# Performance work log

Measured on AMD Instinct MI355X. Metric: run time of the kernel, lower is better.

Reference implementation:

```python
import jax, jax.numpy as jnp
import numpy as np

# GemNet-OC hyperparameters (match init_kwargs)
CUTOFF = 6.0
NR = 128     # num_radial
NS = 7       # num_spherical
NB = 2       # num_blocks
DA = 256     # emb_size_atom
DE = 512     # emb_size_edge
DT = 64      # emb_size_trip
DC = 16      # emb_size_cbf/rbf
NRES_M = 2   # edge residual layers per block (before+after skip)
NRES_H = 2   # atom residual layers per block (num_atom)
N_ELEM = 119
INV_SQRT2 = 0.7071067811865476
_GAMMA = 0.5 / (CUTOFF / NR) ** 2  # gaussian rbf width


def _radial_basis(d):
    """Gaussian RBF with polynomial envelope (exponent 5). d: [E] -> [E, NR]."""
    u = d / CUTOFF
    p = 5.0
    env = 1.0 - (p + 1) * (p + 2) / 2 * u**5 + p * (p + 2) * u**6 - p * (p + 1) / 2 * u**7
    env = jnp.where(u < 1.0, env, 0.0)
    mu = jnp.linspace(0.0, CUTOFF, NR, dtype=d.dtype)
    return env[:, None] * jnp.exp(-_GAMMA * (d[:, None] - mu) ** 2)


def setup_inputs() -> dict:
    key = jax.random.key(0)
    ks = jax.random.split(key, 32)
    N, E, T = 8000, 100000, 500000

    atomic_numbers = jax.random.randint(ks[0], (N,), 0, N_ELEM)
    edge_index = jax.random.randint(ks[1], (2, E), 0, N)
    distances = jax.random.uniform(ks[2], (E,), jnp.float32, 0.5, CUTOFF)
    id3_ba = jax.random.randint(ks[3], (T,), 0, E)
    id3_ca = jax.random.randint(ks[4], (T,), 0, E)
    cos_angles = jax.random.uniform(ks[5], (T,), jnp.float32, -0.99, 0.99)

    def w(k, shape, fan_in):
        return jax.random.normal(k, shape, jnp.float32) / np.sqrt(fan_in)

    params = dict(
        atom_table=w(ks[6], (N_ELEM, DA), 1.0),
        W_edge=w(ks[7], (2 * DA + NR, DE), 2 * DA + NR), b_edge=jnp.zeros((DE,), jnp.float32),
        W_rbf3=w(ks[8], (NR, DC), NR),
        W_sph=w(ks[9], (NS, DC), NS),
        W_cbf_up=w(ks[10], (DC, DT), DC),
        W_rbf_h=w(ks[11], (NR, DE), NR),
        W_ba=w(ks[12], (NB, DE, DE), DE), b_ba=jnp.zeros((NB, DE), jnp.float32),
        W_down=w(ks[13], (NB, DE, DT), DE),
        W_trip_up=w(ks[14], (NB, DT, DE), DT),
        W_res_m=w(ks[15], (NB, NRES_M, 2, DE, DE), DE), b_res_m=jnp.zeros((NB, NRES_M, 2, DE), jnp.float32),
        W_e2a=w(ks[16], (NB, DE, DA), DE),
        W_res_h=w(ks[17], (NB, NRES_H, 2, DA, DA), DA), b_res_h=jnp.zeros((NB, NRES_H, 2, DA), jnp.float32),
        W_out=w(ks[18], (DA, 1), DA),
    )
    return dict(atomic_numbers=atomic_numbers, edge_index=edge_index, distances=distances,
                id3_ba=id3_ba, id3_ca=id3_ca, cos_angles=cos_angles, **params)


def reference(atomic_numbers, edge_index, distances, id3_ba, id3_ca, cos_angles,
              atom_table, W_edge, b_edge, W_rbf3, W_sph, W_cbf_up, W_rbf_h,
              W_ba, b_ba, W_down, W_trip_up, W_res_m, b_res_m, W_e2a,
              W_res_h, b_res_h, W_out):
    N = atomic_numbers.shape[0]
    E = distances.shape[0]
    silu = jax.nn.silu

    # --- shared basis functions ---
    rbf = _radial_basis(distances)                               # [E, NR]
    theta = jnp.arccos(jnp.clip(cos_angles, -1.0, 1.0))
    sph = jnp.cos(theta[:, None] * jnp.arange(NS, dtype=theta.dtype))  # [T, NS]
    # circular basis embedding: radial part (gathered per triplet) x angular part
    cbf_emb = (rbf @ W_rbf3)[id3_ba] * (sph @ W_sph)             # [T, DC]
    cbf_up = cbf_emb @ W_cbf_up                                  # [T, DT]
    rbf_h = rbf @ W_rbf_h                                        # [E, DE]

    # --- embeddings ---
    src, tgt = edge_index[0], edge_index[1]
    h = atom_table[atomic_numbers]                               # [N, DA]
    m = silu(jnp.concatenate([h[src], h[tgt], rbf], axis=-1) @ W_edge + b_edge)  # [E, DE]

    def residual(x, Wr, br):  # Wr: [2, D, D], br: [2, D]
        y = silu(x @ Wr[0] + br[0])
        y = silu(y @ Wr[1] + br[1])
        return (x + y) * INV_SQRT2

    # --- interaction blocks ---
    for b in range(NB):
        # triplet message passing (edge -> triplet gather, triplet -> edge scatter)
        x_ba = silu(m @ W_ba[b] + b_ba[b]) @ W_down[b]           # [E, DT]
        x3 = jax.ops.segment_sum(x_ba[id3_ba] * cbf_up, id3_ca, num_segments=E)  # [E, DT]
        m = (m + x3 @ W_trip_up[b]) * INV_SQRT2
        for r in range(NRES_M):
            m = residual(m, W_res_m[b, r], b_res_m[b, r])
        # atom update: rbf-scaled edge messages scattered onto target atoms
        h_msg = jax.ops.segment_sum((m * rbf_h) @ W_e2a[b], tgt, num_segments=N)  # [N, DA]
        h = h + h_msg
        for r in range(NRES_H):
            h = residual(h, W_res_h[b, r], b_res_h[b, r])

    # --- extensive energy output ---
    energy = jnp.sum(h @ W_out)
    return energy
```

## Files before the change

kernel.cpp:

```cpp
#include <hip/hip_runtime.h>
#include <hip/hip_bf16.h>
#include <math.h>

#define CUTOFF 6.0f
#define NRAD 128
#define NSPH 7
#define DA 256
#define DE 512
#define DT 64
#define DCB 16
#define INV_SQRT2 0.7071067811865476f
#define RBF_GAMMA 227.55555555555554f

typedef __hip_bfloat16 bf16;
typedef __bf16 bf16v;
typedef bf16v bf16x8 __attribute__((ext_vector_type(8)));
typedef float f32x4 __attribute__((ext_vector_type(4)));

static inline int cdiv(int a, int b) { return (a + b - 1) / b; }

__device__ __forceinline__ float silu_f(float v) {
    return v / (1.0f + __expf(-v));
}

__device__ __forceinline__ float to_f(float v) { return v; }
__device__ __forceinline__ float to_f(bf16 v) { return __bfloat162float(v); }

template<typename T> __device__ __forceinline__ T from_f(float v);
template<> __device__ __forceinline__ float from_f<float>(float v) { return v; }
template<> __device__ __forceinline__ bf16 from_f<bf16>(float v) { return __float2bfloat16(v); }

#if defined(__has_builtin)
#if __has_builtin(__builtin_amdgcn_global_load_lds)
#define HAS_GLD 1
#endif
#endif

#ifdef HAS_GLD
__device__ __forceinline__ void gld16(const bf16* g, bf16* l) {
    __builtin_amdgcn_global_load_lds(
        (const __attribute__((address_space(1))) void*)g,
        (__attribute__((address_space(3))) void*)l, 16, 0, 0);
}
#endif

template<typename TC, typename TD, int GMODE, bool PRE_ADD, bool HAS_BIAS,
         bool ACT, bool POST_ADD, bool POST_MUL>
__global__ __launch_bounds__(512, 6)
void gemm_mfma(const bf16* __restrict__ A, const bf16* __restrict__ A3,
               const bf16* __restrict__ Bt,
               TC* __restrict__ C, const TC* __restrict__ Cin,
               const TD* __restrict__ Dop, const float* __restrict__ bias,
               const int* __restrict__ idx1, const int* __restrict__ idx2,
               int M, int N, int K, int lda, int ldb, float scale)
{
    __shared__ bf16 lds[3 * 8192];
    const int tid = threadIdx.x;

    const int nwg = gridDim.x * gridDim.y;
    const int bid = blockIdx.y * gridDim.x + blockIdx.x;
    const int q = nwg >> 3, r = nwg & 7;
    const int xcd = bid & 7, jj = bid >> 3;
    const int wg = (xcd < r) ? (xcd * (q + 1) + jj) : (r + xcd * q + jj);
    const int bn = (wg % gridDim.x) * 128;
    const int bm = (wg / gridDim.x) * 128;

    const int w   = tid >> 6;
    const int l   = tid & 63;
    const int l16 = l & 15;
    const int lr4 = (l >> 4) * 4;
    const int wr  = (w >> 2) * 64;
    const int wc  = (w & 3) * 32;
    const int koff = (((l >> 4) ^ ((l16 >> 1) & 3)) << 3);

    f32x4 acc[4][2];
#pragma unroll
    for (int i = 0; i < 4; ++i)
#pragma unroll
        for (int j = 0; j < 2; ++j) acc[i][j] = (f32x4){0.f, 0.f, 0.f, 0.f};

    const int csw = (((l & 3) ^ ((l >> 3) & 3)) << 3);
    const int rA = w * 16 + (l >> 2);

    int ar = bm + rA; if (ar >= M) ar = M - 1;
    const bf16* pAa = A + (long)((GMODE >= 2) ? idx1[ar] : ar) * lda + csw;
    const bf16* pAb = (GMODE >= 2) ? (A + (long)idx2[ar] * lda + csw) : pAa;
    const bf16* pAc = (GMODE == 3) ? (A3 + (long)ar * NRAD + csw) : pAa;

    int bc = bn + rA; if (bc >= N) bc = N - 1;
    const bf16* pB = Bt + (long)bc * ldb + csw;

    const int wofs = (w * 16) * 32;

    auto STAGE = [&](int k0, int bo) {
        const bf16* a0;
        if (GMODE == 0) {
            a0 = pAa + k0;
        } else if (GMODE == 2) {
            a0 = (k0 >= DA) ? (pAb + (k0 - DA)) : (pAa + k0);
        } else {
            if (k0 >= 2 * DA)  a0 = pAc + (k0 - 2 * DA);
            else if (k0 >= DA) a0 = pAb + (k0 - DA);
            else               a0 = pAa + k0;
        }
#ifdef HAS_GLD
        gld16(a0, lds + bo + wofs);
        gld16(pB + k0, lds + bo + 4096 + wofs);
#else
        *(uint4*)(lds + bo + (tid >> 2) * 32 + (tid & 3) * 8) = *(const uint4*)a0;
        *(uint4*)(lds + bo + 4096 + (tid >> 2) * 32 + (tid & 3) * 8) = *(const uint4*)(pB + k0);
#endif
    };

    auto COMPUTE = [&](int bo) {
        const bf16* As_ = lds + bo;
        const bf16* Bs_ = lds + bo + 4096;
        bf16x8 bfr[2];
#pragma unroll
        for (int fn = 0; fn < 2; ++fn)
            bfr[fn] = *(const bf16x8*)&Bs_[(wc + fn * 16 + l16) * 32 + koff];
#pragma unroll
        for (int fm = 0; fm < 4; ++fm) {
            bf16x8 af = *(const bf16x8*)&As_[(wr + fm * 16 + l16) * 32 + koff];
            acc[fm][0] = __builtin_amdgcn_mfma_f32_16x16x32_bf16(af, bfr[0], acc[fm][0], 0, 0, 0);
            acc[fm][1] = __builtin_amdgcn_mfma_f32_16x16x32_bf16(af, bfr[1], acc[fm][1], 0, 0, 0);
        }
    };

    const int nt = K >> 5;

#ifdef HAS_GLD
    if (nt > 0) STAGE(0, 0);
    if (nt > 1) STAGE(32, 8192);
    int boC = 0;
    int boS = 16384;
    for (int t = 0; t < nt; ++t) {
        if (t + 2 < nt) STAGE((t + 2) << 5, boS);
        const int rem = nt - 1 - t;
        __builtin_amdgcn_sched_barrier(0);
        if (rem >= 2)      asm volatile("s_waitcnt vmcnt(4)" ::: "memory");
        else if (rem == 1) asm volatile("s_waitcnt vmcnt(2)" ::: "memory");
        else               asm volatile("s_waitcnt vmcnt(0)" ::: "memory");
        __builtin_amdgcn_sched_barrier(0);
        __builtin_amdgcn_s_barrier();
        __builtin_amdgcn_sched_barrier(0);
        COMPUTE(boC);
        __builtin_amdgcn_s_barrier();
        boC += 8192; if (boC > 16384) boC = 0;
        boS += 8192; if (boS > 16384) boS = 0;
    }
#else
    for (int t = 0; t < nt; ++t) {
        STAGE(t << 5, 0);
        __syncthreads();
        COMPUTE(0);
        __syncthreads();
    }
#endif

#pragma unroll
    for (int fm = 0; fm < 4; ++fm) {
#pragma unroll
        for (int fn = 0; fn < 2; ++fn) {
            const int col = bn + wc + fn * 16 + l16;
            if (col < N) {
#pragma unroll
                for (int r4 = 0; r4 < 4; ++r4) {
                    const int row = bm + wr + fm * 16 + lr4 + r4;
                    if (row < M) {
                        float v = acc[fm][fn][r4];
                        if (PRE_ADD)  v += to_f(Cin[(long)row * N + col]);
                        if (HAS_BIAS) v += bias[col];
                        if (ACT)      v = silu_f(v);
                        if (POST_ADD) v += to_f(Dop[(long)row * N + col]);
                        if (POST_MUL) v *= to_f(Dop[(long)row * N + col]);
                        C[(long)row * N + col] = from_f<TC>(v * scale);
                    }
                }
            }
        }
    }
}

__global__ void f2b_kernel(const float* __restrict__ in, bf16* __restrict__ out, long n)
{
    long i = ((long)blockIdx.x * 256 + threadIdx.x) * 4;
    const long stride = (long)gridDim.x * 256 * 4;
    for (; i < n; i += stride) {
        float4 v = *(const float4*)(in + i);
        bf16 o[4] = {__float2bfloat16(v.x), __float2bfloat16(v.y),
                     __float2bfloat16(v.z), __float2bfloat16(v.w)};
        *(ushort4*)(out + i) = *(const ushort4*)o;
    }
}

__global__ __launch_bounds__(256)
void t2bT_kernel(const float* __restrict__ in, bf16* __restrict__ out, int K, int Nc)
{
    __shared__ float tile[32][33];
    const long bofs = (long)blockIdx.z * K * Nc;
    const int k0 = blockIdx.y * 32;
    const int n0 = blockIdx.x * 32;
    const int tx = threadIdx.x & 31;
    const int ty = threadIdx.x >> 5;
#pragma unroll
    for (int i = 0; i < 4; ++i) {
        int k = k0 + ty + 8 * i;
        tile[ty + 8 * i][tx] = (k < K && n0 + tx < Nc) ? in[bofs + (long)k * Nc + n0 + tx] : 0.f;
    }
    __syncthreads();
#pragma unroll
    for (int i = 0; i < 4; ++i) {
        int n = n0 + ty + 8 * i;
        if (n < Nc && k0 + tx < K)
            out[bofs + (long)n * K + k0 + tx] = from_f<bf16>(tile[tx][ty + 8 * i]);
    }
}

__global__ __launch_bounds__(128)
void basis_kernel(const float* __restrict__ dist,
                  const float* __restrict__ W_rbf3,
                  bf16* __restrict__ rbf, bf16* __restrict__ rbf3, int E)
{
    __shared__ float s_rbf[NRAD];
    const int e = blockIdx.x;
    if (e >= E) return;
    const int k = threadIdx.x;
    const float d = dist[e];
    const float u = d * (1.0f / CUTOFF);
    float u2 = u * u, u4 = u2 * u2, u5 = u4 * u, u6 = u5 * u, u7 = u6 * u;
    float env = 1.0f - 21.0f * u5 + 35.0f * u6 - 15.0f * u7;
    if (u >= 1.0f) env = 0.0f;
    const float mu = CUTOFF * (float)k / (float)(NRAD - 1);
    const float t = d - mu;
    const float v = env * __expf(-RBF_GAMMA * t * t);
    s_rbf[k] = v;
    rbf[(long)e * NRAD + k] = __float2bfloat16(v);
    __syncthreads();

    if (k < DCB) {
        float acc = 0.f;
        for (int kk = 0; kk < NRAD; ++kk) acc += s_rbf[kk] * W_rbf3[kk * DCB + k];
        rbf3[(long)e * DCB + k] = __float2bfloat16(acc);
    }
}

__global__ void h_init_kernel(const int* __restrict__ an,
                              const float* __restrict__ table,
                              float* __restrict__ h, int N)
{
    int i = blockIdx.x * 256 + threadIdx.x;
    if (i < N * DA) {
        int a = i >> 8;
        int c = i & 255;
        h[i] = table[(long)an[a] * DA + c];
    }
}

__global__ void zeroi_kernel(int* __restrict__ p, int n)
{
    int i = blockIdx.x * 256 + threadIdx.x;
    if (i < n) p[i] = 0;
}
__global__ void copyi_kernel(const int* __restrict__ a, int* __restrict__ b, int n)
{
    int i = blockIdx.x * 256 + threadIdx.x;
    if (i < n) b[i] = a[i];
}
__global__ void count_kernel(const int* __restrict__ idx, int* __restrict__ cnt, int n)
{
    int i = blockIdx.x * 256 + threadIdx.x;
    if (i < n) atomicAdd(&cnt[idx[i]], 1);
}
__global__ __launch_bounds__(256)
void seg_p1(const int* __restrict__ cnt, int* __restrict__ bsum, int n)
{
    __shared__ int s[256];
    int i = blockIdx.x * 256 + threadIdx.x;
    s[threadIdx.x] = (i < n) ? cnt[i] : 0;
    __syncthreads();
    for (int o = 128; o > 0; o >>= 1) {
        if (threadIdx.x < o) s[threadIdx.x] += s[threadIdx.x + o];
        __syncthreads();
    }
    if (threadIdx.x == 0) bsum[blockIdx.x] = s[0];
}
__global__ __launch_bounds__(1024)
void seg_p2(int* __restrict__ bsum, int* __restrict__ off, int nb, int n)
{
    __shared__ int s[1024];
    int v = (threadIdx.x < nb) ? bsum[threadIdx.x] : 0;
    s[threadIdx.x] = v;
    __syncthreads();
    for (int o = 1; o < 1024; o <<= 1) {
        int t = (threadIdx.x >= o) ? s[threadIdx.x - o] : 0;
        __syncthreads();
        s[threadIdx.x] += t;
        __syncthreads();
    }
    if (threadIdx.x < nb) bsum[threadIdx.x] = s[threadIdx.x] - v;
    if (threadIdx.x == nb - 1) off[n] = s[threadIdx.x];
}
__global__ __launch_bounds__(256)
void seg_p3(const int* __restrict__ cnt, const int* __restrict__ bsum,
            int* __restrict__ off, int n)
{
    __shared__ int s[256];
    int i = blockIdx.x * 256 + threadIdx.x;
    int v = (i < n) ? cnt[i] : 0;
    s[threadIdx.x] = v;
    __syncthreads();
    for (int o = 1; o < 256; o <<= 1) {
        int t = (threadIdx.x >= o) ? s[threadIdx.x - o] : 0;
        __syncthreads();
        s[threadIdx.x] += t;
        __syncthreads();
    }
    if (i < n) off[i] = bsum[blockIdx.x] + s[threadIdx.x] - v;
}
__global__ void fill_kernel(const int* __restrict__ idx, int* __restrict__ cur,
                            int* __restrict__ list, int n)
{
    int i = blockIdx.x * 256 + threadIdx.x;
    if (i < n) {
        int p = atomicAdd(&cur[idx[i]], 1);
        list[p] = i;
    }
}

__global__ __launch_bounds__(256)
void emb16_kernel(const float* __restrict__ cosang,
                  const int* __restrict__ id3_ba,
                  const bf16* __restrict__ rbf3,
                  const float* __restrict__ W_sph,
                  bf16* __restrict__ emb, int T)
{
    __shared__ float s_W[NSPH * DCB];
    const int tid = threadIdx.x;
    if (tid < NSPH * DCB) s_W[tid] = W_sph[tid];
    __syncthreads();
    const long idx = (long)blockIdx.x * 256 + tid;
    if (idx >= (long)T * DCB) return;
    const int t = (int)(idx >> 4);
    const int cc = (int)(idx & 15);
    float c = cosang[t];
    c = fminf(1.0f, fmaxf(-1.0f, c));
    float s0 = 1.0f, s1 = c;
    float a = s_W[0 * DCB + cc] + c * s_W[1 * DCB + cc];
#pragma unroll
    for (int s = 2; s < NSPH; ++s) {
        float s2 = 2.0f * c * s1 - s0;
        a += s2 * s_W[s * DCB + cc];
        s0 = s1; s1 = s2;
    }
    emb[idx] = __float2bfloat16(a * to_f(rbf3[(long)id3_ba[t] * DCB + cc]));
}

__global__ __launch_bounds__(256)
void x3_gather_kernel(const int* __restrict__ ca_off, const int* __restrict__ ca_list,
                      const int* __restrict__ id3_ba,
                      const bf16* __restrict__ emb, const bf16* __restrict__ xba,
                      const float* __restrict__ W_up,
                      bf16* __restrict__ x3, int E)
{
    __shared__ float s_Wup[DCB * DT];
    const int tid = threadIdx.x;
    for (int i = tid; i < DCB * DT; i += 256) s_Wup[i] = W_up[i];
    __syncthreads();
    const int e = blockIdx.x * 4 + (tid >> 6);
    const int d = tid & 63;
    if (e >= E) return;
    const int j0 = ca_off[e], j1 = ca_off[e + 1];
    float acc = 0.f;
    for (int j = j0; j < j1; ++j) {
        const int t = ca_list[j];
        const int ba = id3_ba[t];
        const ushort* ep = (const ushort*)(emb + (long)t * DCB);
        float dotv = 0.f;
#pragma unroll
        for (int cc = 0; cc < DCB; ++cc)
            dotv += __uint_as_float((unsigned)ep[cc] << 16) * s_Wup[cc * DT + d];
        acc += dotv * to_f(xba[(long)ba * DT + d]);
    }
    x3[(long)e * DT + d] = from_f<bf16>(acc);
}

__global__ __launch_bounds__(256)
void atom_segsum_kernel(const int* __restrict__ tgt_off, const int* __restrict__ tgt_list,
                        const bf16* __restrict__ g, bf16* __restrict__ s_out, int N)
{
    const int a = blockIdx.x;
    if (a >= N) return;
    const int c = threadIdx.x;
    float acc0 = 0.f, acc1 = 0.f;
    const int j0 = tgt_off[a], j1 = tgt_off[a + 1];
    for (int j = j0; j < j1; ++j) {
        const bf16* row = g + (long)tgt_list[j] * DE;
        acc0 += to_f(row[c]);
        acc1 += to_f(row[c + 256]);
    }
    s_out[(long)a * DE + c]       = from_f<bf16>(acc0);
    s_out[(long)a * DE + c + 256] = from_f<bf16>(acc1);
}

__global__ __launch_bounds__(256)
void reduce1_kernel(const float* __restrict__ h, const float* __restrict__ Wout,
                    float* __restrict__ partials, int N)
{
    __shared__ float s[256];
    const int a0 = blockIdx.x * 32;
    const int col = threadIdx.x;
    float acc = 0.f;
    for (int a = 0; a < 32; ++a) {
        int row = a0 + a;
        if (row < N) acc += h[(long)row * DA + col];
    }
    acc *= Wout[col];
    s[col] = acc;
    __syncthreads();
    for (int off = 128; off > 0; off >>= 1) {
        if (col < off) s[col] += s[col + off];
        __syncthreads();
    }
    if (col == 0) partials[blockIdx.x] = s[0];
}

__global__ __launch_bounds__(256)
void reduce2_kernel(const float* __restrict__ partials, float* __restrict__ out, int nb)
{
    __shared__ float s[256];
    float acc = 0.f;
    for (int i = threadIdx.x; i < nb; i += 256) acc += partials[i];
    s[threadIdx.x] = acc;
    __syncthreads();
    for (int off = 128; off > 0; off >>= 1) {
        if (threadIdx.x < off) s[threadIdx.x] += s[threadIdx.x + off];
        __syncthreads();
    }
    if (threadIdx.x == 0) out[0] = s[0];
}

__global__ void diag_kernel(float* out, float v) { out[0] = v; }

extern "C" void kernel_launch(void* const* d_in, const int* in_sizes, int n_in,
                              void* d_out, int out_size, void* d_ws, size_t ws_size,
                              hipStream_t stream)
{
    const int*   atomic_numbers = (const int*)d_in[0];
    const int*   edge_index     = (const int*)d_in[1];
    const float* distances      = (const float*)d_in[2];
    const int*   id3_ba         = (const int*)d_in[3];
    const int*   id3_ca         = (const int*)d_in[4];
    const float* cos_angles     = (const float*)d_in[5];
    const float* atom_table     = (const float*)d_in[6];
    const float* W_edge         = (const float*)d_in[7];
    const float* b_edge         = (const float*)d_in[8];
    const float* W_rbf3         = (const float*)d_in[9];
    const float* W_sph          = (const float*)d_in[10];
    const float* W_cbf_up       = (const float*)d_in[11];
    const float* W_rbf_h        = (const float*)d_in[12];
    const float* W_ba           = (const float*)d_in[13];
    const float* b_ba           = (const float*)d_in[14];
    const float* W_down         = (const float*)d_in[15];
    const float* W_trip_up      = (const float*)d_in[16];
    const float* W_res_m        = (const float*)d_in[17];
    const float* b_res_m        = (const float*)d_in[18];
    const float* W_e2a          = (const float*)d_in[19];
    const float* W_res_h        = (const float*)d_in[20];
    const float* b_res_h        = (const float*)d_in[21];
    const float* W_out          = (const float*)d_in[22];

    const int N = in_sizes[0];
    const int E = in_sizes[2];
    const int T = in_sizes[3];
    const int* src = edge_index;
    const int* tgt = edge_index + E;

    char* base = (char*)d_ws;
    size_t off = 0;
    auto alloc = [&](size_t bytes) -> void* {
        void* r = base + off;
        off += (bytes + 255) & ~(size_t)255;
        return r;
    };
    bf16*  m     = (bf16*)alloc((size_t)E * DE * 2);
    bf16*  t1    = (bf16*)alloc((size_t)E * DE * 2);
    bf16*  rbf   = (bf16*)alloc((size_t)E * NRAD * 2);
    bf16*  rbf3  = (bf16*)alloc((size_t)E * DCB * 2);
    bf16*  xba   = (bf16*)alloc((size_t)E * DT * 2);
    float* h     = (float*)alloc((size_t)N * DA * 4);
    float* partials = (float*)alloc(4096 * 4);
    bf16* wedgeT = (bf16*)alloc((size_t)DE * (2 * DA + NRAD) * 2);
    bf16* wbaT   = (bf16*)alloc((size_t)2 * DE * DE * 2);
    bf16* wdownT = (bf16*)alloc((size_t)2 * DT * DE * 2);
    bf16* wtripT = (bf16*)alloc((size_t)2 * DE * DT * 2);
    bf16* wresmT = (bf16*)alloc((size_t)8 * DE * DE * 2);
    bf16* we2aT  = (bf16*)alloc((size_t)2 * DA * DE * 2);
    bf16* wrbfhT = (bf16*)alloc((size_t)DE * NRAD * 2);
    bf16* h_bf   = (bf16*)alloc((size_t)N * DA * 2);
    int* tgt_off  = (int*)alloc((size_t)(N + 1) * 4);
    int* tgt_list = (int*)alloc((size_t)E * 4);
    int* ca_off   = (int*)alloc((size_t)(E + 1) * 4);
    int* ca_list  = (int*)alloc((size_t)T * 4);
    bf16*  x3b    = t1;
    bf16*  emb16  = (bf16*)((char*)t1 + 20000000);
    bf16*  wreshT = (bf16*)((char*)t1 + 40000000);
    int*   cur_a  = (int*)t1;
    int*   cur_b  = (int*)((char*)t1 + 4000000);
    int*   bsum   = (int*)((char*)t1 + 8000000);
    bf16*  s_bf   = xba;
    bf16*  tmph_b = xba;

    if (off > ws_size) {
        diag_kernel<<<1, 1, 0, stream>>>((float*)d_out, (float)(ws_size >> 20));
        return;
    }

    const dim3 blk(256);
    const dim3 blk5(512);

    { dim3 g(DE / 32, (2 * DA + NRAD) / 32, 1);
      t2bT_kernel<<<g, blk, 0, stream>>>(W_edge, wedgeT, 2 * DA + NRAD, DE); }
    { dim3 g(DE / 32, DE / 32, 2);
      t2bT_kernel<<<g, blk, 0, stream>>>(W_ba, wbaT, DE, DE); }
    { dim3 g(DT / 32, DE / 32, 2);
      t2bT_kernel<<<g, blk, 0, stream>>>(W_down, wdownT, DE, DT); }
    { dim3 g(DE / 32, DT / 32, 2);
      t2bT_kernel<<<g, blk, 0, stream>>>(W_trip_up, wtripT, DT, DE); }
    { dim3 g(DE / 32, DE / 32, 8);
      t2bT_kernel<<<g, blk, 0, stream>>>(W_res_m, wresmT, DE, DE); }
    { dim3 g(DA / 32, DE / 32, 2);
      t2bT_kernel<<<g, blk, 0, stream>>>(W_e2a, we2aT, DE, DA); }
    { dim3 g(DE / 32, NRAD / 32, 1);
      t2bT_kernel<<<g, blk, 0, stream>>>(W_rbf_h, wrbfhT, NRAD, DE); }

    {
        zeroi_kernel<<<cdiv(N, 256), blk, 0, stream>>>(cur_a, N);
        count_kernel<<<cdiv(E, 256), blk, 0, stream>>>(tgt, cur_a, E);
        seg_p1<<<cdiv(N, 256), blk, 0, stream>>>(cur_a, bsum, N);
        seg_p2<<<1, 1024, 0, stream>>>(bsum, tgt_off, cdiv(N, 256), N);
        seg_p3<<<cdiv(N, 256), blk, 0, stream>>>(cur_a, bsum, tgt_off, N);
        copyi_kernel<<<cdiv(N, 256), blk, 0, stream>>>(tgt_off, cur_a, N);
        fill_kernel<<<cdiv(E, 256), blk, 0, stream>>>(tgt, cur_a, tgt_list, E);
        zeroi_kernel<<<cdiv(E, 256), blk, 0, stream>>>(cur_b, E);
        count_kernel<<<cdiv(T, 256), blk, 0, stream>>>(id3_ca, cur_b, T);
        seg_p1<<<cdiv(E, 256), blk, 0, stream>>>(cur_b, bsum, E);
        seg_p2<<<1, 1024, 0, stream>>>(bsum, ca_off, cdiv(E, 256), E);
        seg_p3<<<cdiv(E, 256), blk, 0, stream>>>(cur_b, bsum, ca_off, E);
        copyi_kernel<<<cdiv(E, 256), blk, 0, stream>>>(ca_off, cur_b, E);
        fill_kernel<<<cdiv(T, 256), blk, 0, stream>>>(id3_ca, cur_b, ca_list, T);
    }

    basis_kernel<<<E, 128, 0, stream>>>(distances, W_rbf3, rbf, rbf3, E);
    h_init_kernel<<<cdiv(N * DA, 256), blk, 0, stream>>>(atomic_numbers, atom_table, h, N);
    f2b_kernel<<<256, blk, 0, stream>>>(h, h_bf, (long)N * DA);

    {
        dim3 g(cdiv(DE, 128), cdiv(E, 128));
        gemm_mfma<bf16, bf16, 3, false, true, true, false, false>
            <<<g, blk5, 0, stream>>>(h_bf, rbf, wedgeT, m, nullptr, nullptr, b_edge,
                                     src, tgt, E, DE, 2 * DA + NRAD, DA, 2 * DA + NRAD, 1.0f);
    }

    for (int b = 0; b < 2; ++b) {
        const bf16* WbaT = wbaT + (long)b * DE * DE;
        const float* bba = b_ba + (long)b * DE;
        const bf16* WdnT = wdownT + (long)b * DT * DE;
        const bf16* WtuT = wtripT + (long)b * DE * DT;
        const bf16* We2aT = we2aT + (long)b * DA * DE;

        {
            dim3 g(cdiv(DE, 128), cdiv(E, 128));
            gemm_mfma<bf16, bf16, 0, false, true, true, false, false>
                <<<g, blk5, 0, stream>>>(m, nullptr, WbaT, t1, nullptr, (const bf16*)nullptr,
                                         bba, nullptr, nullptr, E, DE, DE, DE, DE, 1.0f);
        }
        {
            dim3 g(cdiv(DT, 128), cdiv(E, 128));
            gemm_mfma<bf16, bf16, 0, false, false, false, false, false>
                <<<g, blk5, 0, stream>>>(t1, nullptr, WdnT, xba, nullptr, (const bf16*)nullptr,
                                         nullptr, nullptr, nullptr, E, DT, DE, DE, DE, 1.0f);
        }
        emb16_kernel<<<cdiv(T * DCB, 256), blk, 0, stream>>>(cos_angles, id3_ba, rbf3,
                                                             W_sph, emb16, T);
        x3_gather_kernel<<<cdiv(E, 4), blk, 0, stream>>>(ca_off, ca_list, id3_ba,
                                                         emb16, xba, W_cbf_up, x3b, E);
        {
            dim3 g(cdiv(DE, 128), cdiv(E, 128));
            gemm_mfma<bf16, bf16, 0, true, false, false, false, false>
                <<<g, blk5, 0, stream>>>(x3b, nullptr, WtuT, m, m, (const bf16*)nullptr,
                                         nullptr, nullptr, nullptr, E, DE, DT, DT, DT, INV_SQRT2);
        }
        for (int r = 0; r < 2; ++r) {
            const bf16* W0T = wresmT + (((long)b * 2 + r) * 2 + 0) * DE * DE;
            const bf16* W1T = wresmT + (((long)b * 2 + r) * 2 + 1) * DE * DE;
            const float* b0 = b_res_m + (((long)b * 2 + r) * 2 + 0) * DE;
            const float* b1 = b_res_m + (((long)b * 2 + r) * 2 + 1) * DE;
            dim3 g(cdiv(DE, 128), cdiv(E, 128));
            gemm_mfma<bf16, bf16, 0, false, true, true, false, false>
                <<<g, blk5, 0, stream>>>(m, nullptr, W0T, t1, nullptr, (const bf16*)nullptr,
                                         b0, nullptr, nullptr, E, DE, DE, DE, DE, 1.0f);
            gemm_mfma<bf16, bf16, 0, false, true, true, true, false>
                <<<g, blk5, 0, stream>>>(t1, nullptr, W1T, m, nullptr, m, b1,
                                         nullptr, nullptr, E, DE, DE, DE, DE, INV_SQRT2);
        }
        {
            dim3 g(cdiv(DE, 128), cdiv(E, 128));
            gemm_mfma<bf16, bf16, 0, false, false, false, false, true>
                <<<g, blk5, 0, stream>>>(rbf, nullptr, wrbfhT, t1, nullptr, m, nullptr,
                                         nullptr, nullptr, E, DE, NRAD, NRAD, NRAD, 1.0f);
        }
        atom_segsum_kernel<<<N, blk, 0, stream>>>(tgt_off, tgt_list, t1, s_bf, N);
        {
            dim3 g(cdiv(DA, 128), cdiv(N, 128));
            gemm_mfma<float, float, 0, true, false, false, false, false>
                <<<g, blk5, 0, stream>>>(s_bf, nullptr, We2aT, h, h, (const float*)nullptr,
                                         nullptr, nullptr, nullptr, N, DA, DE, DE, DE, 1.0f);
        }
        {
            dim3 gt(DA / 32, DA / 32, 4);
            t2bT_kernel<<<gt, blk, 0, stream>>>(W_res_h + (long)b * 4 * DA * DA,
                                                wreshT, DA, DA);
        }
        for (int r = 0; r < 2; ++r) {
            const bf16* W0T = wreshT + (long)(r * 2 + 0) * DA * DA;
            const bf16* W1T = wreshT + (long)(r * 2 + 1) * DA * DA;
            const float* b0 = b_res_h + (((long)b * 2 + r) * 2 + 0) * DA;
            const float* b1 = b_res_h + (((long)b * 2 + r) * 2 + 1) * DA;
            f2b_kernel<<<256, blk, 0, stream>>>(h, h_bf, (long)N * DA);
            dim3 g(cdiv(DA, 128), cdiv(N, 128));
            gemm_mfma<bf16, bf16, 0, false, true, true, false, false>
                <<<g, blk5, 0, stream>>>(h_bf, nullptr, W0T, tmph_b, nullptr,
                                         (const bf16*)nullptr, b0, nullptr, nullptr,
                                         N, DA, DA, DA, DA, 1.0f);
            gemm_mfma<float, float, 0, false, true, true, true, false>
                <<<g, blk5, 0, stream>>>(tmph_b, nullptr, W1T, h, nullptr, h, b1,
                                         nullptr, nullptr, N, DA, DA, DA, DA, INV_SQRT2);
        }
    }

    const int nb1 = cdiv(N, 32);
    reduce1_kernel<<<nb1, blk, 0, stream>>>(h, W_out, partials, N);
    reduce2_kernel<<<1, blk, 0, stream>>>(partials, (float*)d_out, nb1);
}
```

Measured before the change: 2.075 ms.

## Add persistent MFMA GEMM that pipelines loads across consecutive M tiles

Adds a persistent GEMM kernel in which each workgroup owns a contiguous run of 128-row M tiles for one N column block. It keeps a triple-buffered global-to-LDS pipeline running continuously across tile boundaries, so prologue and epilogue stalls are amortized and launch-wave tails shrink. The grid is capped at about 768 workgroups. All dense GEMMs except the gathered edge-init GEMM switch to it. The risk is load imbalance across workgroups and the loss of whatever the old kernel's per-tile setup did better.

```diff
diff --git a/kernel.cpp b/kernel.cpp
--- a/kernel.cpp
+++ b/kernel.cpp
@@ -43,6 +43,158 @@
         (__attribute__((address_space(3))) void*)l, 16, 0, 0);
 }
 #endif
+
+template<typename TC, typename TD, bool PRE_ADD, bool HAS_BIAS,
+         bool ACT, bool POST_ADD, bool POST_MUL>
+__global__ __launch_bounds__(512, 6)
+void gemm_pers(const bf16* __restrict__ A, const bf16* __restrict__ Bt,
+               TC* __restrict__ C, const TC* __restrict__ Cin,
+               const TD* __restrict__ Dop, const float* __restrict__ bias,
+               int M, int N, int K, int lda, int ldb, float scale)
+{
+    __shared__ bf16 lds[3 * 8192];
+    const int tid = threadIdx.x;
+
+    const int gx = gridDim.x, gy = gridDim.y;
+    const int nwg = gx * gy;
+    const int bid = blockIdx.y * gx + blockIdx.x;
+    const int q = nwg >> 3, r = nwg & 7;
+    const int xcd = bid & 7, jj = bid >> 3;
+    const int wg = (xcd < r) ? (xcd * (q + 1) + jj) : (r + xcd * q + jj);
+    const int x = wg % gx;
+    const int g = wg / gx;
+    const int bn = x * 128;
+
+    const int KC = K >> 5;
+    const int ntiles = (M + 127) >> 7;
+    const int tq = ntiles / gy, tr = ntiles % gy;
+    const int mt0 = (g < tr) ? g * (tq + 1) : tr * (tq + 1) + (g - tr) * tq;
+    const int npg = (g < tr) ? (tq + 1) : tq;
+    if (npg <= 0) return;
+    const int NS = npg * KC;
+
+    const int w   = tid >> 6;
+    const int l   = tid & 63;
+    const int l16 = l & 15;
+    const int lr4 = (l >> 4) * 4;
+    const int wr  = (w >> 2) * 64;
+    const int wc  = (w & 3) * 32;
+    const int koff = (((l >> 4) ^ ((l16 >> 1) & 3)) << 3);
+
+    f32x4 acc[4][2];
+#pragma unroll
+    for (int i = 0; i < 4; ++i)
+#pragma unroll
+        for (int j = 0; j < 2; ++j) acc[i][j] = (f32x4){0.f, 0.f, 0.f, 0.f};
+
+    const int csw = (((l & 3) ^ ((l >> 3) & 3)) << 3);
+    const int rA = w * 16 + (l >> 2);
+
+    int bc = bn + rA; if (bc >= N) bc = N - 1;
+    const bf16* pB = Bt + (long)bc * ldb + csw;
+
+    const int wofs = (w * 16) * 32;
+
+    auto STAGE = [&](int smt, int skc, int bo) {
+        int ar = (smt << 7) + rA; if (ar >= M) ar = M - 1;
+        const bf16* a0 = A + (long)ar * lda + (skc << 5) + csw;
+#ifdef HAS_GLD
+        gld16(a0, lds + bo + wofs);
+        gld16(pB + (skc << 5), lds + bo + 4096 + wofs);
+#else
+        *(uint4*)(lds + bo + (tid >> 2) * 32 + (tid & 3) * 8) = *(const uint4*)a0;
+        *(uint4*)(lds + bo + 4096 + (tid >> 2) * 32 + (tid & 3) * 8) =
+            *(const uint4*)(pB + (skc << 5));
+#endif
+    };
+
+    auto COMPUTE = [&](int bo) {
+        const bf16* As_ = lds + bo;
+        const bf16* Bs_ = lds + bo + 4096;
+        bf16x8 bfr[2];
+#pragma unroll
+        for (int fn = 0; fn < 2; ++fn)
+            bfr[fn] = *(const bf16x8*)&Bs_[(wc + fn * 16 + l16) * 32 + koff];
+#pragma unroll
+        for (int fm = 0; fm < 4; ++fm) {
+            bf16x8 af = *(const bf16x8*)&As_[(wr + fm * 16 + l16) * 32 + koff];
+            acc[fm][0] = __builtin_amdgcn_mfma_f32_16x16x32_bf16(af, bfr[0], acc[fm][0], 0, 0, 0);
+            acc[fm][1] = __builtin_amdgcn_mfma_f32_16x16x32_bf16(af, bfr[1], acc[fm][1], 0, 0, 0);
+        }
+    };
+
+    auto EPILOGUE = [&](int cmt) {
+        const int bm = cmt << 7;
+#pragma unroll
+        for (int fm = 0; fm < 4; ++fm) {
+#pragma unroll
+            for (int fn = 0; fn < 2; ++fn) {
+                const int col = bn + wc + fn * 16 + l16;
+                if (col < N) {
+#pragma unroll
+                    for (int r4 = 0; r4 < 4; ++r4) {
+                        const int row = bm + wr + fm * 16 + lr4 + r4;
+                        if (row < M) {
+                            float v = acc[fm][fn][r4];
+                            if (PRE_ADD)  v += to_f(Cin[(long)row * N + col]);
+                            if (HAS_BIAS) v += bias[col];
+                            if (ACT)      v = silu_f(v);
+                            if (POST_ADD) v += to_f(Dop[(long)row * N + col]);
+                            if (POST_MUL) v *= to_f(Dop[(long)row * N + col]);
+                            C[(long)row * N + col] = from_f<TC>(v * scale);
+                        }
+                    }
+                }
+                acc[fm][fn] = (f32x4){0.f, 0.f, 0.f, 0.f};
+            }
+        }
+    };
+
+    int smt = mt0, skc = 0;
+    auto ADV_S = [&]() { if (++skc == KC) { skc = 0; ++smt; } };
+
+#ifdef HAS_GLD
+    if (NS > 0) { STAGE(smt, skc, 0);    ADV_S(); }
+    if (NS > 1) { STAGE(smt, skc, 8192); ADV_S(); }
+    int cmt = mt0, ckc = 0;
+    int boC = 0, boS = 16384;
+    for (int s = 0; s < NS; ++s) {
+        if (s + 2 < NS) { STAGE(smt, skc, boS); ADV_S(); }
+        const int rem = NS - 1 - s;
+        __builtin_amdgcn_sched_barrier(0);
+        if (rem >= 2)      asm volatile("s_waitcnt vmcnt(4)" ::: "memory");
+        else if (rem == 1) asm volatile("s_waitcnt vmcnt(2)" ::: "memory");
+        else               asm volatile("s_waitcnt vmcnt(0)" ::: "memory");
+        __builtin_amdgcn_sched_barrier(0);
+        __builtin_amdgcn_s_barrier();
+        __builtin_amdgcn_sched_barrier(0);
+        COMPUTE(boC);
+        __builtin_amdgcn_s_barrier();
+        if (ckc == KC - 1) EPILOGUE(cmt);
+        if (++ckc == KC) { ckc = 0; ++cmt; }
+        boC += 8192; if (boC > 16384) boC = 0;
+        boS += 8192; if (boS > 16384) boS = 0;
+    }
+#else
+    int cmt = mt0, ckc = 0;
+    for (int s = 0; s < NS; ++s) {
+        STAGE(cmt, ckc, 0);
+        __syncthreads();
+        COMPUTE(0);
+        __syncthreads();
+        if (ckc == KC - 1) EPILOGUE(cmt);
+        if (++ckc == KC) { ckc = 0; ++cmt; }
+    }
+#endif
+}
+
+static inline dim3 pers_grid(int M, int N) {
+    int gx = cdiv(N, 128);
+    int ntiles = cdiv(M, 128);
+    int gy = 768 / gx;
+    if (gy > ntiles) gy = ntiles;
+    return dim3(gx, gy);
+}
 
 template<typename TC, typename TD, int GMODE, bool PRE_ADD, bool HAS_BIAS,
          bool ACT, bool POST_ADD, bool POST_MUL>
@@ -569,54 +721,45 @@
         const bf16* WtuT = wtripT + (long)b * DE * DT;
         const bf16* We2aT = we2aT + (long)b * DA * DE;
 
-        {
-            dim3 g(cdiv(DE, 128), cdiv(E, 128));
-            gemm_mfma<bf16, bf16, 0, false, true, true, false, false>
-                <<<g, blk5, 0, stream>>>(m, nullptr, WbaT, t1, nullptr, (const bf16*)nullptr,
-                                         bba, nullptr, nullptr, E, DE, DE, DE, DE, 1.0f);
-        }
-        {
-            dim3 g(cdiv(DT, 128), cdiv(E, 128));
-            gemm_mfma<bf16, bf16, 0, false, false, false, false, false>
-                <<<g, blk5, 0, stream>>>(t1, nullptr, WdnT, xba, nullptr, (const bf16*)nullptr,
-                                         nullptr, nullptr, nullptr, E, DT, DE, DE, DE, 1.0f);
-        }
+        gemm_pers<bf16, bf16, false, true, true, false, false>
+            <<<pers_grid(E, DE), blk5, 0, stream>>>(m, WbaT, t1, (const bf16*)nullptr,
+                                                    (const bf16*)nullptr, bba,
+                                                    E, DE, DE, DE, DE, 1.0f);
+        gemm_pers<bf16, bf16, false, false, false, false, false>
+            <<<pers_grid(E, DT), blk5, 0, stream>>>(t1, WdnT, xba, (const bf16*)nullptr,
+                                                    (const bf16*)nullptr, nullptr,
+                                                    E, DT, DE, DE, DE, 1.0f);
         emb16_kernel<<<cdiv(T * DCB, 256), blk, 0, stream>>>(cos_angles, id3_ba, rbf3,
                                                              W_sph, emb16, T);
         x3_gather_kernel<<<cdiv(E, 4), blk, 0, stream>>>(ca_off, ca_list, id3_ba,
                                                          emb16, xba, W_cbf_up, x3b, E);
-        {
-            dim3 g(cdiv(DE, 128), cdiv(E, 128));
-            gemm_mfma<bf16, bf16, 0, true, false, false, false, false>
-                <<<g, blk5, 0, stream>>>(x3b, nullptr, WtuT, m, m, (const bf16*)nullptr,
-                                         nullptr, nullptr, nullptr, E, DE, DT, DT, DT, INV_SQRT2);
-        }
+        gemm_pers<bf16, bf16, true, false, false, false, false>
+            <<<pers_grid(E, DE), blk5, 0, stream>>>(x3b, WtuT, m, m,
+                                                    (const bf16*)nullptr, nullptr,
+                                                    E, DE, DT, DT, DT, INV_SQRT2);
         for (int r = 0; r < 2; ++r) {
             const bf16* W0T = wresmT + (((long)b * 2 + r) * 2 + 0) * DE * DE;
             const bf16* W1T = wresmT + (((long)b * 2 + r) * 2 + 1) * DE * DE;
             const float* b0 = b_res_m + (((long)b * 2 + r) * 2 + 0) * DE;
             const float* b1 = b_res_m + (((long)b * 2 + r) * 2 + 1) * DE;
-            dim3 g(cdiv(DE, 128), cdiv(E, 128));
-            gemm_mfma<bf16, bf16, 0, false, true, true, false, false>
-                <<<g, blk5, 0, stream>>>(m, nullptr, W0T, t1, nullptr, (const bf16*)nullptr,
-                                         b0, nullptr, nullptr, E, DE, DE, DE, DE, 1.0f);
-            gemm_mfma<bf16, bf16, 0, false, true, true, true, false>
-                <<<g, blk5, 0, stream>>>(t1, nullptr, W1T, m, nullptr, m, b1,
-                                         nullptr, nullptr, E, DE, DE, DE, DE, INV_SQRT2);
+            gemm_pers<bf16, bf16, false, true, true, false, false>
+                <<<pers_grid(E, DE), blk5, 0, stream>>>(m, W0T, t1, (const bf16*)nullptr,
+                                                        (const bf16*)nullptr, b0,
+                                                        E, DE, DE, DE, DE, 1.0f);
+            gemm_pers<bf16, bf16, false, true, true, true, false>
+                <<<pers_grid(E, DE), blk5, 0, stream>>>(t1, W1T, m, (const bf16*)nullptr,
+                                                        m, b1,
+                                                        E, DE, DE, DE, DE, INV_SQRT2);
         }
-        {
-            dim3 g(cdiv(DE, 128), cdiv(E, 128));
-            gemm_mfma<bf16, bf16, 0, false, false, false, false, true>
-                <<<g, blk5, 0, stream>>>(rbf, nullptr, wrbfhT, t1, nullptr, m, nullptr,
-                                         nullptr, nullptr, E, DE, NRAD, NRAD, NRAD, 1.0f);
-        }
+        gemm_pers<bf16, bf16, false, false, false, false, true>
+            <<<pers_grid(E, DE), blk5, 0, stream>>>(rbf, wrbfhT, t1, (const bf16*)nullptr,
+                                                    m, nullptr,
+                                                    E, DE, NRAD, NRAD, NRAD, 1.0f);
         atom_segsum_kernel<<<N, blk, 0, stream>>>(tgt_off, tgt_list, t1, s_bf, N);
-        {
-            dim3 g(cdiv(DA, 128), cdiv(N, 128));
-            gemm_mfma<float, float, 0, true, false, false, false, false>
-                <<<g, blk5, 0, stream>>>(s_bf, nullptr, We2aT, h, h, (const float*)nullptr,
-                                         nullptr, nullptr, nullptr, N, DA, DE, DE, DE, 1.0f);
-        }
+        gemm_pers<float, float, true, false, false, false, false>
+            <<<pers_grid(N, DA), blk5, 0, stream>>>(s_bf, We2aT, h, h,
+                                                    (const float*)nullptr, nullptr,
+                                                    N, DA, DE, DE, DE, 1.0f);
         {
             dim3 gt(DA / 32, DA / 32, 4);
             t2bT_kernel<<<gt, blk, 0, stream>>>(W_res_h + (long)b * 4 * DA * DA,
@@ -628,14 +771,15 @@
             const float* b0 = b_res_h + (((long)b * 2 + r) * 2 + 0) * DA;
             const float* b1 = b_res_h + (((long)b * 2 + r) * 2 + 1) * DA;
             f2b_kernel<<<256, blk, 0, stream>>>(h, h_bf, (long)N * DA);
-            dim3 g(cdiv(DA, 128), cdiv(N, 128));
-            gemm_mfma<bf16, bf16, 0, false, true, true, false, false>
-                <<<g, blk5, 0, stream>>>(h_bf, nullptr, W0T, tmph_b, nullptr,
-                                         (const bf16*)nullptr, b0, nullptr, nullptr,
-                                         N, DA, DA, DA, DA, 1.0f);
-            gemm_mfma<float, float, 0, false, true, true, true, false>
-                <<<g, blk5, 0, stream>>>(tmph_b, nullptr, W1T, h, nullptr, h, b1,
-                                         nullptr, nullptr, N, DA, DA, DA, DA, INV_SQRT2);
+            gemm_pers<bf16, bf16, false, true, true, false, false>
+                <<<pers_grid(N, DA), blk5, 0, stream>>>(h_bf, W0T, tmph_b,
+                                                        (const bf16*)nullptr,
+                                                        (const bf16*)nullptr, b0,
+                                                        N, DA, DA, DA, DA, 1.0f);
+            gemm_pers<float, float, false, true, true, true, false>
+                <<<pers_grid(N, DA), blk5, 0, stream>>>(tmph_b, W1T, h,
+                                                        (const float*)nullptr, h, b1,
+                                                        N, DA, DA, DA, DA, INV_SQRT2);
         }
     }
 
```

Result: slower. 2.159 ms (+4.1%).
